# Optimization experiments

Hardware: AMD Instinct MI355X
Metric: run time of the kernel (lower is better)

Reference implementation:

```python
import jax, jax.numpy as jnp
import numpy as np

B, T, H, E = 256, 256, 512, 96  # batch, enc seq len, hidden/enc dim, charset size


def setup_inputs() -> dict:
    key = jax.random.key(0)
    ks = jax.random.split(key, 9)
    s = 0.05  # param scale
    return {
        "prev_h": jax.random.normal(ks[0], (B, H), jnp.float32),
        "prev_c": jax.random.normal(ks[1], (B, H), jnp.float32),
        "batch_H": jax.random.normal(ks[2], (B, T, H), jnp.float32),
        "char_onehots": jax.nn.one_hot(jax.random.randint(ks[3], (B,), 0, E), E, dtype=jnp.float32),
        "W_i2h": jax.random.normal(ks[4], (H, H), jnp.float32) * s,
        "W_h2h": jax.random.normal(ks[5], (H, H), jnp.float32) * s,
        "b_h2h": jnp.zeros((H,), jnp.float32),
        "w_score": jax.random.normal(ks[6], (H, 1), jnp.float32) * s,
        "W_lstm": jax.random.normal(ks[7], (H + E, 4 * H), jnp.float32) * s,
        "U_lstm": jax.random.normal(ks[8], (H, 4 * H), jnp.float32) * s,
        "b_lstm": jnp.zeros((4 * H,), jnp.float32),
    }


def reference(prev_h, prev_c, batch_H, char_onehots,
              W_i2h, W_h2h, b_h2h, w_score, W_lstm, U_lstm, b_lstm):
    # Additive (Bahdanau) attention
    proj = jnp.einsum('btd,dh->bth', batch_H, W_i2h)          # [B,T,H]
    hp = prev_h @ W_h2h + b_h2h                               # [B,H]
    e = jnp.tanh(proj + hp[:, None, :]) @ w_score             # [B,T,1]
    alpha = jax.nn.softmax(e, axis=1)                         # [B,T,1]
    context = jnp.einsum('bt,btd->bd', alpha[..., 0], batch_H)  # [B,D]
    x = jnp.concatenate([context, char_onehots], axis=1)      # [B,D+E]
    # Keras LSTMCell: gate order i, f, c(g), o
    z = x @ W_lstm + prev_h @ U_lstm + b_lstm                 # [B,4H]
    i, f, g, o = jnp.split(z, 4, axis=1)
    c_new = jax.nn.sigmoid(f) * prev_c + jax.nn.sigmoid(i) * jnp.tanh(g)
    h_new = jax.nn.sigmoid(o) * jnp.tanh(c_new)
    return h_new, c_new, alpha
```

## Files before the change

kernel.cpp:

```cpp
#include <hip/hip_runtime.h>
#include <hip/hip_bf16.h>
#include <math.h>

#define Bq 256
#define Tq 256
#define Hq 512
#define Eq 96

typedef __attribute__((ext_vector_type(8))) short short8;
typedef __attribute__((ext_vector_type(4))) float f32x4;

static __device__ __forceinline__ unsigned short f2bf(float f) {
  union { float f; unsigned u; } v; v.f = f;
  unsigned r = v.u + 0x7FFF + ((v.u >> 16) & 1);
  return (unsigned short)(r >> 16);
}

static __device__ __forceinline__ float sat_tanh(float x) {
  float ax = fminf(fabsf(x), 15.0f);
  float e = __builtin_exp2f(ax * 2.885390082f);
  float t = 1.0f - 2.0f / (e + 1.0f);
  return copysignf(t, x);
}

static __device__ __forceinline__ float sat_sig(float x) {
  float cx = fmaxf(fminf(x, 30.0f), -30.0f);
  return 1.0f / (1.0f + __builtin_exp2f(-cx * 1.442695041f));
}

__global__ __launch_bounds__(256) void convW_k(const float* __restrict__ W,
                                               unsigned short* __restrict__ Wt) {
  __shared__ float tile[32][33];
  int bx = blockIdx.x & 15, by = blockIdx.x >> 4;
  int tx = threadIdx.x & 31, ty = threadIdx.x >> 5;
  #pragma unroll
  for (int i = 0; i < 32; i += 8)
    tile[ty + i][tx] = W[(size_t)(by * 32 + ty + i) * Hq + bx * 32 + tx];
  __syncthreads();
  #pragma unroll
  for (int i = 0; i < 32; i += 8)
    Wt[(size_t)(bx * 32 + ty + i) * Hq + by * 32 + tx] = f2bf(tile[tx][ty + i]);
}

__global__ __launch_bounds__(256) void hproj2_k(const float* __restrict__ ph,
                                                const float* __restrict__ Whh,
                                                const float* __restrict__ bh,
                                                float* __restrict__ hp) {
  __shared__ __align__(16) float xs[8][Hq];
  int bg = blockIdx.x >> 2;
  int nc = blockIdx.x & 3;
  int tid = threadIdx.x;
  for (int i = tid; i < 8 * Hq / 4; i += 256)
    ((float4*)&xs[0][0])[i] = ((const float4*)(ph + (size_t)bg * 8 * Hq))[i];
  __syncthreads();
  int rt = tid >> 6;
  int ct = tid & 63;
  int n = nc * 128 + ct * 2;
  float a00 = 0, a01 = 0, a10 = 0, a11 = 0;
  for (int d = 0; d < Hq; d += 4) {
    float4 x0 = *(const float4*)&xs[rt * 2][d];
    float4 x1 = *(const float4*)&xs[rt * 2 + 1][d];
    #pragma unroll
    for (int j = 0; j < 4; j++) {
      float2 w = *(const float2*)&Whh[(size_t)(d + j) * Hq + n];
      float xj0 = ((const float*)&x0)[j];
      float xj1 = ((const float*)&x1)[j];
      a00 += xj0 * w.x; a01 += xj0 * w.y;
      a10 += xj1 * w.x; a11 += xj1 * w.y;
    }
  }
  float b0 = bh[n], b1 = bh[n + 1];
  int row = bg * 8 + rt * 2;
  hp[(size_t)row * Hq + n] = a00 + b0;
  hp[(size_t)row * Hq + n + 1] = a01 + b1;
  hp[(size_t)(row + 1) * Hq + n] = a10 + b0;
  hp[(size_t)(row + 1) * Hq + n + 1] = a11 + b1;
}

#define BM 128
#define BN 128
#define BK 32
#define LDK 40

__global__ __launch_bounds__(256) void fused_score_k(
    const float* __restrict__ A,
    const unsigned short* __restrict__ Wt,
    const float* __restrict__ hp,
    const float* __restrict__ wsc,
    float* __restrict__ e) {
  __shared__ unsigned short As[BM * LDK];
  __shared__ unsigned short Bs[BN * LDK];
  __shared__ float hps[BN];
  __shared__ float wss[BN];

  const int tid = threadIdx.x;
  const int m0 = blockIdx.x * BM;
  const int n0 = blockIdx.y * BN;
  const int bb = m0 >> 8;

  if (tid < BN) {
    hps[tid] = hp[(size_t)bb * Hq + n0 + tid];
    wss[tid] = wsc[n0 + tid];
  }

  const int wave = tid >> 6;
  const int lane = tid & 63;
  const int quad = lane >> 4;
  const int l16 = lane & 15;
  const int wm = (wave & 1) * 64;
  const int wn = (wave >> 1) * 64;

  f32x4 acc[4][4] = {};

  const int arow = tid >> 3;
  const int acol = (tid & 7) * 4;
  const int brow = tid >> 2;
  const int bkh = (tid & 3) * 8;

  for (int k0 = 0; k0 < Hq; k0 += BK) {
    __syncthreads();
    #pragma unroll
    for (int p = 0; p < 4; p++) {
      int r = arow + p * 32;
      const float4 v = *(const float4*)(&A[(size_t)(m0 + r) * Hq + k0 + acol]);
      ushort4 pk;
      pk.x = f2bf(v.x); pk.y = f2bf(v.y); pk.z = f2bf(v.z); pk.w = f2bf(v.w);
      *(ushort4*)&As[r * LDK + acol] = pk;
    }
    #pragma unroll
    for (int p = 0; p < 2; p++) {
      int r = brow + p * 64;
      const uint4 v = *(const uint4*)(&Wt[(size_t)(n0 + r) * Hq + k0 + bkh]);
      *(uint4*)&Bs[r * LDK + bkh] = v;
    }
    __syncthreads();

    short8 af[4], bfr[4];
    #pragma unroll
    for (int mi = 0; mi < 4; mi++)
      af[mi] = *(const short8*)&As[(wm + mi * 16 + l16) * LDK + quad * 8];
    #pragma unroll
    for (int ni = 0; ni < 4; ni++)
      bfr[ni] = *(const short8*)&Bs[(wn + ni * 16 + l16) * LDK + quad * 8];
    #pragma unroll
    for (int mi = 0; mi < 4; mi++)
      #pragma unroll
      for (int ni = 0; ni < 4; ni++)
        acc[mi][ni] = __builtin_amdgcn_mfma_f32_16x16x32_bf16(
            af[mi], bfr[ni], acc[mi][ni], 0, 0, 0);
  }

  float hv[4], wv[4];
  #pragma unroll
  for (int ni = 0; ni < 4; ni++) {
    int c = wn + ni * 16 + l16;
    hv[ni] = hps[c];
    wv[ni] = wss[c];
  }
  #pragma unroll
  for (int mi = 0; mi < 4; mi++) {
    float s[4] = {0, 0, 0, 0};
    #pragma unroll
    for (int ni = 0; ni < 4; ni++)
      #pragma unroll
      for (int r = 0; r < 4; r++)
        s[r] += sat_tanh(acc[mi][ni][r] + hv[ni]) * wv[ni];
    #pragma unroll
    for (int r = 0; r < 4; r++) {
      s[r] += __shfl_xor(s[r], 8, 64);
      s[r] += __shfl_xor(s[r], 4, 64);
      s[r] += __shfl_xor(s[r], 2, 64);
      s[r] += __shfl_xor(s[r], 1, 64);
    }
    if (l16 == 0) {
      int row = m0 + wm + mi * 16 + quad * 4;
      #pragma unroll
      for (int r = 0; r < 4; r++) atomicAdd(&e[row + r], s[r]);
    }
  }
}

__global__ __launch_bounds__(256) void softmax_k(float* __restrict__ ea) {
  __shared__ float red[8];
  int b = blockIdx.x, t = threadIdx.x;
  int wave = t >> 6, lane = t & 63;
  float x = ea[b * Tq + t];
  float m = x;
  #pragma unroll
  for (int off = 32; off >= 1; off >>= 1) m = fmaxf(m, __shfl_xor(m, off, 64));
  if (lane == 0) red[wave] = m;
  __syncthreads();
  m = fmaxf(fmaxf(red[0], red[1]), fmaxf(red[2], red[3]));
  float ex = __builtin_exp2f((x - m) * 1.442695041f);
  float s = ex;
  #pragma unroll
  for (int off = 32; off >= 1; off >>= 1) s += __shfl_xor(s, off, 64);
  if (lane == 0) red[4 + wave] = s;
  __syncthreads();
  s = red[4] + red[5] + red[6] + red[7];
  ea[b * Tq + t] = ex / s;
}

__global__ __launch_bounds__(256) void context_k(const float* __restrict__ alpha,
                                                 const float* __restrict__ bH,
                                                 float* __restrict__ ctx) {
  __shared__ float al[Tq];
  int b = blockIdx.x, tid = threadIdx.x;
  al[tid] = alpha[b * Tq + tid];
  __syncthreads();
  const float2* Hp = (const float2*)(bH + (size_t)b * Tq * Hq);
  float ax = 0.f, ay = 0.f;
  #pragma unroll 4
  for (int t = 0; t < Tq; t++) {
    float a = al[t];
    float2 v = Hp[t * (Hq / 2) + tid];
    ax += a * v.x;
    ay += a * v.y;
  }
  float2 o; o.x = ax; o.y = ay;
  ((float2*)(ctx + (size_t)b * Hq))[tid] = o;
}

#define KXc 1120
__global__ __launch_bounds__(256) void zgates2_k(
    const float* __restrict__ ctx, const float* __restrict__ oneh,
    const float* __restrict__ ph, const float* __restrict__ pc,
    const float* __restrict__ Wl, const float* __restrict__ Ul,
    const float* __restrict__ bl,
    float* __restrict__ outh, float* __restrict__ outc) {
  __shared__ __align__(16) float xs[8 * KXc];
  const int bg = blockIdx.x >> 3;
  const int hc = blockIdx.x & 7;
  const int tid = threadIdx.x;
  const int row0 = bg * 8;

  for (int i = tid; i < 8 * 128; i += 256) {
    int r = i >> 7, dd = (i & 127) * 4;
    *(float4*)&xs[r * KXc + dd] = *(const float4*)&ctx[(size_t)(row0 + r) * Hq + dd];
  }
  for (int i = tid; i < 8 * 128; i += 256) {
    int r = i >> 7, dd = (i & 127) * 4;
    *(float4*)&xs[r * KXc + 608 + dd] = *(const float4*)&ph[(size_t)(row0 + r) * Hq + dd];
  }
  if (tid < 8 * 24) {
    int r = tid / 24, dd = (tid % 24) * 4;
    *(float4*)&xs[r * KXc + 512 + dd] = *(const float4*)&oneh[(row0 + r) * Eq + dd];
  }
  __syncthreads();

  const int rt = tid >> 6;
  const int ct = tid & 63;
  const int c0 = ct * 4;
  const int gate = c0 >> 6;
  const int ho = c0 & 63;
  const int n = gate * 512 + hc * 64 + ho;

  float acc0[4] = {0, 0, 0, 0};
  float acc1[4] = {0, 0, 0, 0};
  const float* xr0 = &xs[(rt * 2) * KXc];
  const float* xr1 = &xs[(rt * 2 + 1) * KXc];

  for (int d = 0; d < 608; d += 4) {
    float4 x0 = *(const float4*)&xr0[d];
    float4 x1 = *(const float4*)&xr1[d];
    #pragma unroll
    for (int j = 0; j < 4; j++) {
      float4 w = *(const float4*)&Wl[(size_t)(d + j) * 2048 + n];
      float a = ((const float*)&x0)[j], b = ((const float*)&x1)[j];
      acc0[0] += a * w.x; acc0[1] += a * w.y; acc0[2] += a * w.z; acc0[3] += a * w.w;
      acc1[0] += b * w.x; acc1[1] += b * w.y; acc1[2] += b * w.z; acc1[3] += b * w.w;
    }
  }
  for (int d = 0; d < 512; d += 4) {
    float4 x0 = *(const float4*)&xr0[608 + d];
    float4 x1 = *(const float4*)&xr1[608 + d];
    #pragma unroll
    for (int j = 0; j < 4; j++) {
      float4 w = *(const float4*)&Ul[(size_t)(d + j) * 2048 + n];
      float a = ((const float*)&x0)[j], b = ((const float*)&x1)[j];
      acc0[0] += a * w.x; acc0[1] += a * w.y; acc0[2] += a * w.z; acc0[3] += a * w.w;
      acc1[0] += b * w.x; acc1[1] += b * w.y; acc1[2] += b * w.z; acc1[3] += b * w.w;
    }
  }

  __syncthreads();
  float* zs = xs;
  #pragma unroll
  for (int j = 0; j < 4; j++) {
    zs[(rt * 2) * 256 + c0 + j] = acc0[j];
    zs[(rt * 2 + 1) * 256 + c0 + j] = acc1[j];
  }
  __syncthreads();

  #pragma unroll
  for (int p = tid; p < 512; p += 256) {
    int r = p >> 6, o = p & 63;
    int h = hc * 64 + o;
    int grow = row0 + r;
    float gi = zs[r * 256 + o]       + bl[h];
    float gf = zs[r * 256 + 64 + o]  + bl[512 + h];
    float gg = zs[r * 256 + 128 + o] + bl[1024 + h];
    float go = zs[r * 256 + 192 + o] + bl[1536 + h];
    float cn = sat_sig(gf) * pc[(size_t)grow * Hq + h] + sat_sig(gi) * sat_tanh(gg);
    float hn = sat_sig(go) * sat_tanh(cn);
    outh[(size_t)grow * Hq + h] = hn;
    outc[(size_t)grow * Hq + h] = cn;
  }
}

extern "C" void kernel_launch(void* const* d_in, const int* in_sizes, int n_in,
                              void* d_out, int out_size, void* d_ws, size_t ws_size,
                              hipStream_t stream) {
  const float* prev_h = (const float*)d_in[0];
  const float* prev_c = (const float*)d_in[1];
  const float* batch_H = (const float*)d_in[2];
  const float* oneh = (const float*)d_in[3];
  const float* W_i2h = (const float*)d_in[4];
  const float* W_h2h = (const float*)d_in[5];
  const float* b_h2h = (const float*)d_in[6];
  const float* w_score = (const float*)d_in[7];
  const float* W_lstm = (const float*)d_in[8];
  const float* U_lstm = (const float*)d_in[9];
  const float* b_lstm = (const float*)d_in[10];

  float* out = (float*)d_out;
  float* outh = out;
  float* outc = out + Bq * Hq;
  float* alpha = out + 2 * Bq * Hq;

  float* ws = (float*)d_ws;
  float* hp = ws;
  float* ctx = ws;
  unsigned short* Wt = (unsigned short*)(ws + 131072);

  hipMemsetAsync(alpha, 0, Bq * Tq * sizeof(float), stream);
  convW_k<<<256, 256, 0, stream>>>(W_i2h, Wt);
  hproj2_k<<<128, 256, 0, stream>>>(prev_h, W_h2h, b_h2h, hp);
  dim3 g2(512, 4);
  fused_score_k<<<g2, 256, 0, stream>>>(batch_H, Wt, hp, w_score, alpha);
  softmax_k<<<256, 256, 0, stream>>>(alpha);
  context_k<<<256, 256, 0, stream>>>(alpha, batch_H, ctx);
  zgates2_k<<<256, 256, 0, stream>>>(ctx, oneh, prev_h, prev_c,
                                     W_lstm, U_lstm, b_lstm, outh, outc);
}
```

Baseline: 486.0 us.

## Split-K the small GEMV-like kernels with atomic accumulation for more parallelism

The hidden projection, context reduction and LSTM gate matmul are split along their reduction dimension into four chunks each, raising grid sizes from 128/256 blocks to 512/1024. Partial sums are combined with float atomicAdd into zeroed workspace buffers. The h2h bias moves into the score kernel, and a separate elementwise kernel applies the gate nonlinearities when the workspace is large enough. This targets low occupancy on a large GPU, at the cost of extra memsets, atomics, an additional launch and nondeterministic summation order.

After: 399.1 us. 1.22x faster.

```diff
diff --git a/kernel.cpp b/kernel.cpp
--- a/kernel.cpp
+++ b/kernel.cpp
@@ -42,39 +42,42 @@
     Wt[(size_t)(bx * 32 + ty + i) * Hq + by * 32 + tx] = f2bf(tile[tx][ty + i]);
 }
 
-__global__ __launch_bounds__(256) void hproj2_k(const float* __restrict__ ph,
+__global__ __launch_bounds__(256) void hsplit_k(const float* __restrict__ ph,
                                                 const float* __restrict__ Whh,
-                                                const float* __restrict__ bh,
                                                 float* __restrict__ hp) {
-  __shared__ __align__(16) float xs[8][Hq];
-  int bg = blockIdx.x >> 2;
-  int nc = blockIdx.x & 3;
-  int tid = threadIdx.x;
-  for (int i = tid; i < 8 * Hq / 4; i += 256)
-    ((float4*)&xs[0][0])[i] = ((const float4*)(ph + (size_t)bg * 8 * Hq))[i];
-  __syncthreads();
-  int rt = tid >> 6;
-  int ct = tid & 63;
-  int n = nc * 128 + ct * 2;
+  __shared__ __align__(16) float xs[8][128];
+  const int ks = blockIdx.x & 3;
+  const int nc = (blockIdx.x >> 2) & 3;
+  const int bg = blockIdx.x >> 4;
+  const int tid = threadIdx.x;
+  const int row0 = bg * 8;
+  const int d0 = ks * 128;
+  for (int i = tid; i < 8 * 32; i += 256) {
+    int r = i >> 5, dd = (i & 31) * 4;
+    *(float4*)&xs[r][dd] = *(const float4*)&ph[(size_t)(row0 + r) * Hq + d0 + dd];
+  }
+  __syncthreads();
+  const int rt = tid >> 6;
+  const int ct = tid & 63;
+  const int n = nc * 128 + ct * 2;
   float a00 = 0, a01 = 0, a10 = 0, a11 = 0;
-  for (int d = 0; d < Hq; d += 4) {
-    float4 x0 = *(const float4*)&xs[rt * 2][d];
-    float4 x1 = *(const float4*)&xs[rt * 2 + 1][d];
+  for (int dd = 0; dd < 128; dd += 4) {
+    float4 x0 = *(const float4*)&xs[rt * 2][dd];
+    float4 x1 = *(const float4*)&xs[rt * 2 + 1][dd];
     #pragma unroll
     for (int j = 0; j < 4; j++) {
-      float2 w = *(const float2*)&Whh[(size_t)(d + j) * Hq + n];
+      float2 w = *(const float2*)&Whh[(size_t)(d0 + dd + j) * Hq + n];
       float xj0 = ((const float*)&x0)[j];
       float xj1 = ((const float*)&x1)[j];
       a00 += xj0 * w.x; a01 += xj0 * w.y;
       a10 += xj1 * w.x; a11 += xj1 * w.y;
     }
   }
-  float b0 = bh[n], b1 = bh[n + 1];
-  int row = bg * 8 + rt * 2;
-  hp[(size_t)row * Hq + n] = a00 + b0;
-  hp[(size_t)row * Hq + n + 1] = a01 + b1;
-  hp[(size_t)(row + 1) * Hq + n] = a10 + b0;
-  hp[(size_t)(row + 1) * Hq + n + 1] = a11 + b1;
+  int row = row0 + rt * 2;
+  atomicAdd(&hp[(size_t)row * Hq + n], a00);
+  atomicAdd(&hp[(size_t)row * Hq + n + 1], a01);
+  atomicAdd(&hp[(size_t)(row + 1) * Hq + n], a10);
+  atomicAdd(&hp[(size_t)(row + 1) * Hq + n + 1], a11);
 }
 
 #define BM 128
@@ -86,6 +89,7 @@
     const float* __restrict__ A,
     const unsigned short* __restrict__ Wt,
     const float* __restrict__ hp,
+    const float* __restrict__ bh,
     const float* __restrict__ wsc,
     float* __restrict__ e) {
   __shared__ unsigned short As[BM * LDK];
@@ -99,7 +103,7 @@
   const int bb = m0 >> 8;
 
   if (tid < BN) {
-    hps[tid] = hp[(size_t)bb * Hq + n0 + tid];
+    hps[tid] = hp[(size_t)bb * Hq + n0 + tid] + bh[n0 + tid];
     wss[tid] = wsc[n0 + tid];
   }
 
@@ -201,24 +205,104 @@
   ea[b * Tq + t] = ex / s;
 }
 
-__global__ __launch_bounds__(256) void context_k(const float* __restrict__ alpha,
-                                                 const float* __restrict__ bH,
-                                                 float* __restrict__ ctx) {
-  __shared__ float al[Tq];
-  int b = blockIdx.x, tid = threadIdx.x;
-  al[tid] = alpha[b * Tq + tid];
-  __syncthreads();
-  const float2* Hp = (const float2*)(bH + (size_t)b * Tq * Hq);
+__global__ __launch_bounds__(256) void ctxsplit_k(const float* __restrict__ alpha,
+                                                  const float* __restrict__ bH,
+                                                  float* __restrict__ ctx) {
+  __shared__ float al[64];
+  const int b = blockIdx.x >> 2;
+  const int tc = blockIdx.x & 3;
+  const int tid = threadIdx.x;
+  if (tid < 64) al[tid] = alpha[b * Tq + tc * 64 + tid];
+  __syncthreads();
+  const float2* Hp = (const float2*)(bH + (size_t)b * Tq * Hq + (size_t)tc * 64 * Hq);
   float ax = 0.f, ay = 0.f;
-  #pragma unroll 4
-  for (int t = 0; t < Tq; t++) {
+  #pragma unroll 8
+  for (int t = 0; t < 64; t++) {
     float a = al[t];
     float2 v = Hp[t * (Hq / 2) + tid];
     ax += a * v.x;
     ay += a * v.y;
   }
-  float2 o; o.x = ax; o.y = ay;
-  ((float2*)(ctx + (size_t)b * Hq))[tid] = o;
+  atomicAdd(&ctx[(size_t)b * Hq + 2 * tid], ax);
+  atomicAdd(&ctx[(size_t)b * Hq + 2 * tid + 1], ay);
+}
+
+__global__ __launch_bounds__(256) void zsplit_k(
+    const float* __restrict__ ctx, const float* __restrict__ oneh,
+    const float* __restrict__ ph, const float* __restrict__ Wl,
+    const float* __restrict__ Ul, float* __restrict__ z) {
+  __shared__ __align__(16) float xs[8 * 280];
+  const int ks = blockIdx.x & 3;
+  const int hc = (blockIdx.x >> 2) & 7;
+  const int bg = blockIdx.x >> 5;
+  const int tid = threadIdx.x;
+  const int row0 = bg * 8;
+  const int dbase = ks * 280;
+
+  for (int i = tid; i < 8 * 280; i += 256) {
+    int r = i / 280, dd = i % 280;
+    int g = dbase + dd;
+    float v;
+    if (g < 512) v = ctx[(size_t)(row0 + r) * Hq + g];
+    else if (g < 608) v = oneh[(row0 + r) * Eq + (g - 512)];
+    else v = ph[(size_t)(row0 + r) * Hq + (g - 608)];
+    xs[r * 280 + dd] = v;
+  }
+  __syncthreads();
+
+  const int rt = tid >> 6;
+  const int ct = tid & 63;
+  const int c0 = ct * 4;
+  const int gate = c0 >> 6;
+  const int ho = c0 & 63;
+  const int n = gate * 512 + hc * 64 + ho;
+
+  float acc0[4] = {0, 0, 0, 0};
+  float acc1[4] = {0, 0, 0, 0};
+  const float* xr0 = &xs[(rt * 2) * 280];
+  const float* xr1 = &xs[(rt * 2 + 1) * 280];
+
+  for (int dd = 0; dd < 280; dd += 4) {
+    float4 x0 = *(const float4*)&xr0[dd];
+    float4 x1 = *(const float4*)&xr1[dd];
+    #pragma unroll
+    for (int j = 0; j < 4; j++) {
+      int d = dbase + dd + j;
+      const float* wp = (d < 608) ? &Wl[(size_t)d * 2048 + n]
+                                  : &Ul[(size_t)(d - 608) * 2048 + n];
+      float4 w = *(const float4*)wp;
+      float a = ((const float*)&x0)[j], b = ((const float*)&x1)[j];
+      acc0[0] += a * w.x; acc0[1] += a * w.y; acc0[2] += a * w.z; acc0[3] += a * w.w;
+      acc1[0] += b * w.x; acc1[1] += b * w.y; acc1[2] += b * w.z; acc1[3] += b * w.w;
+    }
+  }
+  const int r0 = row0 + rt * 2;
+  #pragma unroll
+  for (int j = 0; j < 4; j++) {
+    atomicAdd(&z[(size_t)r0 * 2048 + n + j], acc0[j]);
+    atomicAdd(&z[(size_t)(r0 + 1) * 2048 + n + j], acc1[j]);
+  }
+}
+
+__global__ __launch_bounds__(256) void gatesz_k(const float* __restrict__ z,
+                                                const float* __restrict__ bl,
+                                                const float* __restrict__ pc,
+                                                float* __restrict__ outh,
+                                                float* __restrict__ outc) {
+  int p = blockIdx.x * 256 + threadIdx.x;
+  #pragma unroll
+  for (int q = 0; q < 2; q++, p += 65536) {
+    int r = p >> 9, h = p & 511;
+    const float* zb = z + (size_t)r * 2048;
+    float gi = zb[h] + bl[h];
+    float gf = zb[512 + h] + bl[512 + h];
+    float gg = zb[1024 + h] + bl[1024 + h];
+    float go = zb[1536 + h] + bl[1536 + h];
+    float cn = sat_sig(gf) * pc[p] + sat_sig(gi) * sat_tanh(gg);
+    float hn = sat_sig(go) * sat_tanh(cn);
+    outh[p] = hn;
+    outc[p] = cn;
+  }
 }
 
 #define KXc 1120
@@ -332,14 +416,26 @@
   float* hp = ws;
   float* ctx = ws;
   unsigned short* Wt = (unsigned short*)(ws + 131072);
+  float* z = ws + 131072;
+
+  const bool bigws = ws_size >= 2621440;
 
   hipMemsetAsync(alpha, 0, Bq * Tq * sizeof(float), stream);
+  hipMemsetAsync(hp, 0, Bq * Hq * sizeof(float), stream);
   convW_k<<<256, 256, 0, stream>>>(W_i2h, Wt);
-  hproj2_k<<<128, 256, 0, stream>>>(prev_h, W_h2h, b_h2h, hp);
+  hsplit_k<<<512, 256, 0, stream>>>(prev_h, W_h2h, hp);
   dim3 g2(512, 4);
-  fused_score_k<<<g2, 256, 0, stream>>>(batch_H, Wt, hp, w_score, alpha);
+  fused_score_k<<<g2, 256, 0, stream>>>(batch_H, Wt, hp, b_h2h, w_score, alpha);
   softmax_k<<<256, 256, 0, stream>>>(alpha);
-  context_k<<<256, 256, 0, stream>>>(alpha, batch_H, ctx);
-  zgates2_k<<<256, 256, 0, stream>>>(ctx, oneh, prev_h, prev_c,
-                                     W_lstm, U_lstm, b_lstm, outh, outc);
-}
+  if (bigws) {
+    hipMemsetAsync(ws, 0, 2621440, stream);
+    ctxsplit_k<<<1024, 256, 0, stream>>>(alpha, batch_H, ctx);
+    zsplit_k<<<1024, 256, 0, stream>>>(ctx, oneh, prev_h, W_lstm, U_lstm, z);
+    gatesz_k<<<256, 256, 0, stream>>>(z, b_lstm, prev_c, outh, outc);
+  } else {
+    hipMemsetAsync(ctx, 0, Bq * Hq * sizeof(float), stream);
+    ctxsplit_k<<<1024, 256, 0, stream>>>(alpha, batch_H, ctx);
+    zgates2_k<<<256, 256, 0, stream>>>(ctx, oneh, prev_h, prev_c,
+                                       W_lstm, U_lstm, b_lstm, outh, outc);
+  }
+}
```
